# Kernel optimization log

Hardware: AMD Instinct MI355X
Metric: run time of the kernel (lower is better)

The kernel has to match this reference:

```python
import jax, jax.numpy as jnp
import numpy as np

EPS = 1e-7
TWO_PI = 2.0 * np.pi

K = 4096   # num gaussians
R = 8192   # num rays
MAP_SIZE = 100


def setup_inputs() -> dict:
    key = jax.random.key(0)
    k1, k2, k3, k4, k5, k6 = jax.random.split(key, 6)
    pos_raw = jax.random.normal(k1, (K, 2), dtype=jnp.float32)            # pre-sigmoid positions
    conc_raw = jax.random.normal(k2, (K,), dtype=jnp.float32)             # pre-softplus concentration
    scale_raw = 0.1 * jax.random.normal(k3, (K, 2), dtype=jnp.float32)    # log-scales
    rot_raw = jax.random.uniform(k4, (K,), dtype=jnp.float32) * TWO_PI    # rotation angles
    p_rays = jax.random.uniform(k5, (R, 2), dtype=jnp.float32) * MAP_SIZE # ray origins in map coords
    u = jax.random.normal(k6, (R, 2), dtype=jnp.float32)
    u_rays = u / jnp.linalg.norm(u, axis=-1, keepdims=True)               # unit ray directions
    return {"pos_raw": pos_raw, "conc_raw": conc_raw, "scale_raw": scale_raw,
            "rot_raw": rot_raw, "p_rays": p_rays, "u_rays": u_rays,
            "map_size": MAP_SIZE}


def _forward(pos_raw, conc_raw, scale_raw, rot_raw, p_rays, u_rays, map_size):
    # --- per-gaussian activations (GasSplattingModel getters) ---
    pos = jax.nn.sigmoid(pos_raw) * map_size           # (K,2)
    conc = jax.nn.softplus(conc_raw)                   # (K,)
    scale = jnp.exp(scale_raw)                         # (K,2)
    d0 = 1.0 / (scale[:, 0] ** 2 + EPS)                # diag of S^2 inverse
    d1 = 1.0 / (scale[:, 1] ** 2 + EPS)
    c, s = jnp.cos(rot_raw), jnp.sin(rot_raw)
    # Sigma^{-1} = R diag(d0,d1) R^T with R = [[c,-s],[s,c]]  (symmetric 2x2)
    m00 = c * c * d0 + s * s * d1                      # (K,)
    m01 = c * s * (d0 - d1)
    m11 = s * s * d0 + c * c * d1
    M = jnp.stack([m00, m01, m11], axis=0)             # (3,K) quadratic-form coeffs

    u0, u1 = u_rays[:, 0], u_rays[:, 1]
    p0, p1 = p_rays[:, 0], p_rays[:, 1]

    # quadratic-form features per ray, contracted with M via GEMM -> (R,K)
    qu = jnp.stack([u0 * u0, 2.0 * u0 * u1, u1 * u1], axis=1)        # (R,3)
    qp = jnp.stack([p0 * p0, 2.0 * p0 * p1, p1 * p1], axis=1)        # (R,3)
    qup = jnp.stack([u0 * p0, u0 * p1 + u1 * p0, u1 * p1], axis=1)   # (R,3)
    a = qu @ M          # u^T S u      (R,K)
    pSp = qp @ M        # p^T S p      (R,K)
    uSp = qup @ M       # u^T S p      (R,K)

    # S @ mu per gaussian -> (2,K)
    Sm = jnp.stack([m00 * pos[:, 0] + m01 * pos[:, 1],
                    m01 * pos[:, 0] + m11 * pos[:, 1]], axis=0)
    uSm = u_rays @ Sm   # u^T S mu     (R,K)
    pSm = p_rays @ Sm   # p^T S mu     (R,K)
    mSm = pos[:, 0] * Sm[0] + pos[:, 1] * Sm[1]        # mu^T S mu (K,)

    b = uSp - uSm                                      # u^T S (p - mu)
    c0 = pSp - 2.0 * pSm + mSm[None, :]                # (p-mu)^T S (p-mu)

    # closed-form line integral of conc * exp(-0.5 (x-mu)^T S (x-mu)) along ray
    dens = conc[None, :] * jnp.sqrt(TWO_PI / a) * jnp.exp(-0.5 * (c0 - b * b / a))
    return jnp.sum(dens, axis=-1)                      # (R,)


def reference(pos_raw, conc_raw, scale_raw, rot_raw, p_rays, u_rays, map_size):
    return _forward(pos_raw, conc_raw, scale_raw, rot_raw, p_rays, u_rays, map_size)
```

## Files before the change

### kernel.cpp

```cpp
#include <hip/hip_runtime.h>
#include <hip/hip_bf16.h>

#define EPS 1e-07f

#define BLOCK 1024
#define RPB   32
#define NW    (BLOCK/64)

#define SQRT_HALF_LOG2E 0.84932180028801904f
#define LOG2_SQRT_2PI   1.32574806473616588f

typedef float v4f __attribute__((ext_vector_type(4)));

__global__ __launch_bounds__(BLOCK) void fused_splat(
        const float* __restrict__ pos_raw,
        const float* __restrict__ conc_raw,
        const float* __restrict__ scale_raw,
        const float* __restrict__ rot_raw,
        const void*  __restrict__ map_size_p,
        const float* __restrict__ p_rays,
        const float* __restrict__ u_rays,
        float* __restrict__ out,
        int K, int R)
{
    __shared__ float sG[512][6][4];
    __shared__ float psum[NW][RPB];

    const int tid  = threadIdx.x;
    const int lane = tid & 63;
    const int wv   = tid >> 6;
    const int rayl = lane & 31;
    const int half = lane >> 5;
    const int chunk = (wv << 1) | half;

    int ray = blockIdx.x * RPB + rayl;
    if (ray >= R) ray = R - 1;

    unsigned int msbits = *(const unsigned int*)map_size_p;
    float msf = __uint_as_float(msbits);
    const float ms = (msf >= 1e-3f && msf <= 1e9f) ? msf
                                                   : (float)(*(const int*)map_size_p);

    float2 p2 = *(const float2*)(p_rays + 2*ray);
    float2 u2 = *(const float2*)(u_rays + 2*ray);
    const float p0 = p2.x, p1 = p2.y, u0 = u2.x, u1 = u2.y;
    const float qu0  = u0*u0, qu1 = 2.0f*u0*u1, qu2 = u1*u1;
    const float wt   =  SQRT_HALF_LOG2E * (u0*p1 - u1*p0);
    const float su1  =  SQRT_HALF_LOG2E * u1;
    const float nsu0 = -SQRT_HALF_LOG2E * u0;

    float acc = 0.0f;

    const int KH = K >> 1;
    const int CL = KH >> 5;
    const int NG = CL >> 2;

    for (int pass = 0; pass < 2; ++pass) {
        const int kbase = pass * KH;

        __syncthreads();

        for (int k = tid; k < KH; k += BLOCK) {
            const int kg = kbase + k;

            float pr0 = pos_raw[2*kg], pr1 = pos_raw[2*kg+1];
            float pos0 = ms / (1.0f + __expf(-pr0));
            float pos1 = ms / (1.0f + __expf(-pr1));

            float cr = conc_raw[kg];
            float conc = fmaxf(cr, 0.0f) + __logf(1.0f + __expf(-fabsf(cr)));

            float s0 = __expf(scale_raw[2*kg]);
            float s1 = __expf(scale_raw[2*kg+1]);
            float d0 = 1.0f / (s0*s0 + EPS);
            float d1 = 1.0f / (s1*s1 + EPS);

            float rot = rot_raw[kg];
            float c = __cosf(rot), s = __sinf(rot);

            float m00 = c*c*d0 + s*s*d1;
            float m01 = c*s*(d0 - d1);
            float m11 = s*s*d0 + c*c*d1;

            float det    = d0 * d1;
            float invdet = 1.0f / det;
            float cc = __log2f(conc) + LOG2_SQRT_2PI - 0.5f * __log2f(det);

            const int q = k >> 2, e = k & 3;
            sG[q][0][e] = m00 * invdet;
            sG[q][1][e] = m01 * invdet;
            sG[q][2][e] = m11 * invdet;
            sG[q][3][e] = cc;
            sG[q][4][e] = pos0;
            sG[q][5][e] = pos1;
        }
        __syncthreads();

        const int g0 = chunk * NG;
        #pragma unroll 4
        for (int gq = 0; gq < NG; ++gq) {
            const int t4 = g0 + gq;
            v4f M00 = *(const v4f*)&sG[t4][0][0];
            v4f M01 = *(const v4f*)&sG[t4][1][0];
            v4f M11 = *(const v4f*)&sG[t4][2][0];
            v4f CC  = *(const v4f*)&sG[t4][3][0];
            v4f P0  = *(const v4f*)&sG[t4][4][0];
            v4f P1  = *(const v4f*)&sG[t4][5][0];

            #pragma unroll
            for (int g = 0; g < 4; ++g) {
                float a_  = fmaf(qu2, M11[g], fmaf(qu1, M01[g], qu0 * M00[g]));
                float cr_ = fmaf(nsu0, P1[g], fmaf(su1, P0[g], wt));
                float ra_ = __builtin_amdgcn_rsqf(a_);
                float t_  = cr_ * ra_;
                float ar_ = fmaf(-t_, t_, CC[g]);
                float e_  = __builtin_amdgcn_exp2f(ar_);
                acc = fmaf(ra_, e_, acc);
            }
        }
    }

    acc += __shfl_xor(acc, 32, 64);
    if (half == 0) psum[wv][rayl] = acc;
    __syncthreads();

    if (wv == 0 && lane < RPB) {
        float s = 0.0f;
        #pragma unroll
        for (int w = 0; w < NW; ++w) s += psum[w][lane];
        int oray = blockIdx.x * RPB + lane;
        if (oray < R) out[oray] = s;
    }
}

extern "C" void kernel_launch(void* const* d_in, const int* in_sizes, int n_in,
                              void* d_out, int out_size, void* d_ws, size_t ws_size,
                              hipStream_t stream)
{
    const float* pos_raw   = (const float*)d_in[0];
    const float* conc_raw  = (const float*)d_in[1];
    const float* scale_raw = (const float*)d_in[2];
    const float* rot_raw   = (const float*)d_in[3];
    const float* p_rays    = (const float*)d_in[4];
    const float* u_rays    = (const float*)d_in[5];
    const void*  map_size  = d_in[6];

    const int K = in_sizes[1];
    const int R = out_size;

    float* out = (float*)d_out;

    dim3 grid((R + RPB - 1) / RPB);
    fused_splat<<<grid, BLOCK, 0, stream>>>(pos_raw, conc_raw, scale_raw,
                                            rot_raw, map_size,
                                            p_rays, u_rays, out, K, R);
}
```

Measured before the change: 21.03 us.

## Split into precompute kernel and scalar-load splat kernel with K-chunk atomics

The per-gaussian activations move into a separate precompute kernel that writes a padded 4-wide record layout to the workspace and zeroes the output. The main kernel gives one ray per thread, splits K across 64 grid-y chunks, and reads gaussian records through inline-asm scalar loads (s_load) instead of LDS, finishing with an atomicAdd per ray. This removes the per-block redundant activation work, the __syncthreads and the LDS traffic. In exchange it adds a second launch, global atomics, and a full wait on every scalar load that serializes load latency with compute.

```diff
diff --git a/kernel.cpp b/kernel.cpp
--- a/kernel.cpp
+++ b/kernel.cpp
@@ -3,47 +3,94 @@
 
 #define EPS 1e-07f
 
-#define BLOCK 1024
-#define RPB   32
-#define NW    (BLOCK/64)
+#define BLOCK  256
+#define NCH    64
+#define PBLOCK 64
 
 #define SQRT_HALF_LOG2E 0.84932180028801904f
 #define LOG2_SQRT_2PI   1.32574806473616588f
 
 typedef float v4f __attribute__((ext_vector_type(4)));
 
-__global__ __launch_bounds__(BLOCK) void fused_splat(
-        const float* __restrict__ pos_raw,
-        const float* __restrict__ conc_raw,
-        const float* __restrict__ scale_raw,
-        const float* __restrict__ rot_raw,
-        const void*  __restrict__ map_size_p,
-        const float* __restrict__ p_rays,
-        const float* __restrict__ u_rays,
-        float* __restrict__ out,
-        int K, int R)
+__global__ __launch_bounds__(PBLOCK) void precompute_gauss(
+                                 const float* __restrict__ pos_raw,
+                                 const float* __restrict__ conc_raw,
+                                 const float* __restrict__ scale_raw,
+                                 const float* __restrict__ rot_raw,
+                                 const void*  __restrict__ map_size_p,
+                                 float* __restrict__ gG,
+                                 float* __restrict__ out,
+                                 int K, int KPAD, int R)
 {
-    __shared__ float sG[512][6][4];
-    __shared__ float psum[NW][RPB];
+    int k = blockIdx.x * blockDim.x + threadIdx.x;
+    int nthreads = gridDim.x * blockDim.x;
 
-    const int tid  = threadIdx.x;
-    const int lane = tid & 63;
-    const int wv   = tid >> 6;
-    const int rayl = lane & 31;
-    const int half = lane >> 5;
-    const int chunk = (wv << 1) | half;
+    for (int i = k; i < R; i += nthreads) out[i] = 0.0f;
 
-    int ray = blockIdx.x * RPB + rayl;
-    if (ray >= R) ray = R - 1;
+    if (k >= KPAD) return;
+
+    const int q = k >> 2, e = k & 3;
+    float* rec = gG + q * 24;
+
+    if (k >= K) {
+        rec[0  + e] = 1.0f;
+        rec[4  + e] = 0.0f;
+        rec[8  + e] = 1.0f;
+        rec[12 + e] = -1e38f;
+        rec[16 + e] = 0.0f;
+        rec[20 + e] = 0.0f;
+        return;
+    }
 
     unsigned int msbits = *(const unsigned int*)map_size_p;
     float msf = __uint_as_float(msbits);
     const float ms = (msf >= 1e-3f && msf <= 1e9f) ? msf
                                                    : (float)(*(const int*)map_size_p);
 
-    float2 p2 = *(const float2*)(p_rays + 2*ray);
-    float2 u2 = *(const float2*)(u_rays + 2*ray);
+    float pr0 = pos_raw[2*k],  pr1 = pos_raw[2*k+1];
+    float pos0 = ms / (1.0f + __expf(-pr0));
+    float pos1 = ms / (1.0f + __expf(-pr1));
+
+    float cr = conc_raw[k];
+    float conc = fmaxf(cr, 0.0f) + __logf(1.0f + __expf(-fabsf(cr)));
+
+    float s0 = __expf(scale_raw[2*k]);
+    float s1 = __expf(scale_raw[2*k+1]);
+    float d0 = 1.0f / (s0*s0 + EPS);
+    float d1 = 1.0f / (s1*s1 + EPS);
+
+    float rot = rot_raw[k];
+    float c = __cosf(rot), s = __sinf(rot);
+
+    float m00 = c*c*d0 + s*s*d1;
+    float m01 = c*s*(d0 - d1);
+    float m11 = s*s*d0 + c*c*d1;
+
+    float det    = d0 * d1;
+    float invdet = 1.0f / det;
+    float cc = __log2f(conc) + LOG2_SQRT_2PI - 0.5f * __log2f(det);
+
+    rec[0  + e] = m00 * invdet;
+    rec[4  + e] = m01 * invdet;
+    rec[8  + e] = m11 * invdet;
+    rec[12 + e] = cc;
+    rec[16 + e] = pos0;
+    rec[20 + e] = pos1;
+}
+
+__global__ __launch_bounds__(BLOCK) void splat_main(
+        const float* __restrict__ p_rays,
+        const float* __restrict__ u_rays,
+        const float* __restrict__ gG,
+        float* __restrict__ out,
+        int GPC, int R)
+{
+    const int ray = blockIdx.x * BLOCK + threadIdx.x;
+
+    float2 p2 = *(const float2*)(p_rays + 2*min(ray, R-1));
+    float2 u2 = *(const float2*)(u_rays + 2*min(ray, R-1));
     const float p0 = p2.x, p1 = p2.y, u0 = u2.x, u1 = u2.y;
+
     const float qu0  = u0*u0, qu1 = 2.0f*u0*u1, qu2 = u1*u1;
     const float wt   =  SQRT_HALF_LOG2E * (u0*p1 - u1*p0);
     const float su1  =  SQRT_HALF_LOG2E * u1;
@@ -51,86 +98,36 @@
 
     float acc = 0.0f;
 
-    const int KH = K >> 1;
-    const int CL = KH >> 5;
-    const int NG = CL >> 2;
+    const float* gptr = gG + (size_t)blockIdx.y * GPC * 24;
 
-    for (int pass = 0; pass < 2; ++pass) {
-        const int kbase = pass * KH;
+    for (int g = 0; g < GPC; ++g) {
+        v4f M00, M01, M11, CC, P0, P1;
+        asm volatile(
+            "s_load_dwordx4 %0, %6, 0x0\n\t"
+            "s_load_dwordx4 %1, %6, 0x10\n\t"
+            "s_load_dwordx4 %2, %6, 0x20\n\t"
+            "s_load_dwordx4 %3, %6, 0x30\n\t"
+            "s_load_dwordx4 %4, %6, 0x40\n\t"
+            "s_load_dwordx4 %5, %6, 0x50\n\t"
+            "s_waitcnt lgkmcnt(0)"
+            : "=&s"(M00), "=&s"(M01), "=&s"(M11),
+              "=&s"(CC),  "=&s"(P0),  "=&s"(P1)
+            : "s"(gptr));
 
-        __syncthreads();
-
-        for (int k = tid; k < KH; k += BLOCK) {
-            const int kg = kbase + k;
-
-            float pr0 = pos_raw[2*kg], pr1 = pos_raw[2*kg+1];
-            float pos0 = ms / (1.0f + __expf(-pr0));
-            float pos1 = ms / (1.0f + __expf(-pr1));
-
-            float cr = conc_raw[kg];
-            float conc = fmaxf(cr, 0.0f) + __logf(1.0f + __expf(-fabsf(cr)));
-
-            float s0 = __expf(scale_raw[2*kg]);
-            float s1 = __expf(scale_raw[2*kg+1]);
-            float d0 = 1.0f / (s0*s0 + EPS);
-            float d1 = 1.0f / (s1*s1 + EPS);
-
-            float rot = rot_raw[kg];
-            float c = __cosf(rot), s = __sinf(rot);
-
-            float m00 = c*c*d0 + s*s*d1;
-            float m01 = c*s*(d0 - d1);
-            float m11 = s*s*d0 + c*c*d1;
-
-            float det    = d0 * d1;
-            float invdet = 1.0f / det;
-            float cc = __log2f(conc) + LOG2_SQRT_2PI - 0.5f * __log2f(det);
-
-            const int q = k >> 2, e = k & 3;
-            sG[q][0][e] = m00 * invdet;
-            sG[q][1][e] = m01 * invdet;
-            sG[q][2][e] = m11 * invdet;
-            sG[q][3][e] = cc;
-            sG[q][4][e] = pos0;
-            sG[q][5][e] = pos1;
+        #pragma unroll
+        for (int e = 0; e < 4; ++e) {
+            float a_  = fmaf(qu2, M11[e], fmaf(qu1, M01[e], qu0 * M00[e]));
+            float cr_ = fmaf(nsu0, P1[e], fmaf(su1, P0[e], wt));
+            float ra_ = __builtin_amdgcn_rsqf(a_);
+            float t_  = cr_ * ra_;
+            float ar_ = fmaf(-t_, t_, CC[e]);
+            float e_  = __builtin_amdgcn_exp2f(ar_);
+            acc = fmaf(ra_, e_, acc);
         }
-        __syncthreads();
-
-        const int g0 = chunk * NG;
-        #pragma unroll 4
-        for (int gq = 0; gq < NG; ++gq) {
-            const int t4 = g0 + gq;
-            v4f M00 = *(const v4f*)&sG[t4][0][0];
-            v4f M01 = *(const v4f*)&sG[t4][1][0];
-            v4f M11 = *(const v4f*)&sG[t4][2][0];
-            v4f CC  = *(const v4f*)&sG[t4][3][0];
-            v4f P0  = *(const v4f*)&sG[t4][4][0];
-            v4f P1  = *(const v4f*)&sG[t4][5][0];
-
-            #pragma unroll
-            for (int g = 0; g < 4; ++g) {
-                float a_  = fmaf(qu2, M11[g], fmaf(qu1, M01[g], qu0 * M00[g]));
-                float cr_ = fmaf(nsu0, P1[g], fmaf(su1, P0[g], wt));
-                float ra_ = __builtin_amdgcn_rsqf(a_);
-                float t_  = cr_ * ra_;
-                float ar_ = fmaf(-t_, t_, CC[g]);
-                float e_  = __builtin_amdgcn_exp2f(ar_);
-                acc = fmaf(ra_, e_, acc);
-            }
-        }
+        gptr += 24;
     }
 
-    acc += __shfl_xor(acc, 32, 64);
-    if (half == 0) psum[wv][rayl] = acc;
-    __syncthreads();
-
-    if (wv == 0 && lane < RPB) {
-        float s = 0.0f;
-        #pragma unroll
-        for (int w = 0; w < NW; ++w) s += psum[w][lane];
-        int oray = blockIdx.x * RPB + lane;
-        if (oray < R) out[oray] = s;
-    }
+    if (ray < R) atomicAdd(&out[ray], acc);
 }
 
 extern "C" void kernel_launch(void* const* d_in, const int* in_sizes, int n_in,
@@ -148,10 +145,22 @@
     const int K = in_sizes[1];
     const int R = out_size;
 
+    const int ng_tot = (K + 3) / 4;
+    const int GPC    = (ng_tot + NCH - 1) / NCH;
+    const int ng_pad = GPC * NCH;
+    const int KPAD   = ng_pad * 4;
+
     float* out = (float*)d_out;
+    float* gG  = (float*)d_ws;
 
-    dim3 grid((R + RPB - 1) / RPB);
-    fused_splat<<<grid, BLOCK, 0, stream>>>(pos_raw, conc_raw, scale_raw,
-                                            rot_raw, map_size,
-                                            p_rays, u_rays, out, K, R);
+    {
+        dim3 grid((KPAD + PBLOCK - 1) / PBLOCK);
+        precompute_gauss<<<grid, PBLOCK, 0, stream>>>(pos_raw, conc_raw, scale_raw,
+                                                      rot_raw, map_size,
+                                                      gG, out, K, KPAD, R);
+    }
+    {
+        dim3 grid((R + BLOCK - 1) / BLOCK, NCH);
+        splat_main<<<grid, BLOCK, 0, stream>>>(p_rays, u_rays, gG, out, GPC, R);
+    }
 }
```

After: 23.56 us. +12.0%, slower.

## Halve rays per block, split gaussians across 64 chunks with padded LDS records

Applied to the files above, without the earlier changes.

Rays per block drop from 32 to 16, so each wave covers 4 chunks of 16 rays and the block splits gaussians into 64 chunks of 32 per pass. The shared-memory layout is regrouped into padded per-chunk records with a 196-float stride, meant to avoid LDS bank conflicts. The inner loop keeps four independent accumulators for ILP, and a launch-bounds occupancy hint is added. The trade-off is twice as many blocks, so per-block gaussian preprocessing is repeated twice as often, plus an extra shuffle step in the reduction.

```diff
diff --git a/kernel.cpp b/kernel.cpp
--- a/kernel.cpp
+++ b/kernel.cpp
@@ -4,7 +4,10 @@
 #define EPS 1e-07f
 
 #define BLOCK 1024
-#define RPB   32
+#define RPB   16
+#define NCHK  64
+#define GPG   8
+#define CSTRIDE 196
 #define NW    (BLOCK/64)
 
 #define SQRT_HALF_LOG2E 0.84932180028801904f
@@ -12,7 +15,7 @@
 
 typedef float v4f __attribute__((ext_vector_type(4)));
 
-__global__ __launch_bounds__(BLOCK) void fused_splat(
+__global__ __launch_bounds__(BLOCK, 8) void fused_splat(
         const float* __restrict__ pos_raw,
         const float* __restrict__ conc_raw,
         const float* __restrict__ scale_raw,
@@ -23,15 +26,14 @@
         float* __restrict__ out,
         int K, int R)
 {
-    __shared__ float sG[512][6][4];
+    __shared__ float sG[NCHK * CSTRIDE];
     __shared__ float psum[NW][RPB];
 
-    const int tid  = threadIdx.x;
-    const int lane = tid & 63;
-    const int wv   = tid >> 6;
-    const int rayl = lane & 31;
-    const int half = lane >> 5;
-    const int chunk = (wv << 1) | half;
+    const int tid   = threadIdx.x;
+    const int lane  = tid & 63;
+    const int wv    = tid >> 6;
+    const int rayl  = tid & (RPB - 1);
+    const int chunk = tid >> 4;
 
     int ray = blockIdx.x * RPB + rayl;
     if (ray >= R) ray = R - 1;
@@ -49,11 +51,10 @@
     const float su1  =  SQRT_HALF_LOG2E * u1;
     const float nsu0 = -SQRT_HALF_LOG2E * u0;
 
-    float acc = 0.0f;
+    float acc0 = 0.0f, acc1 = 0.0f, acc2 = 0.0f, acc3 = 0.0f;
 
     const int KH = K >> 1;
-    const int CL = KH >> 5;
-    const int NG = CL >> 2;
+    const float* cb = &sG[chunk * CSTRIDE];
 
     for (int pass = 0; pass < 2; ++pass) {
         const int kbase = pass * KH;
@@ -87,41 +88,58 @@
             float cc = __log2f(conc) + LOG2_SQRT_2PI - 0.5f * __log2f(det);
 
             const int q = k >> 2, e = k & 3;
-            sG[q][0][e] = m00 * invdet;
-            sG[q][1][e] = m01 * invdet;
-            sG[q][2][e] = m11 * invdet;
-            sG[q][3][e] = cc;
-            sG[q][4][e] = pos0;
-            sG[q][5][e] = pos1;
+            float* rec = &sG[(q >> 3) * CSTRIDE + (q & 7) * 24];
+            rec[ 0 + e] = m00 * invdet;
+            rec[ 4 + e] = m01 * invdet;
+            rec[ 8 + e] = m11 * invdet;
+            rec[12 + e] = cc;
+            rec[16 + e] = pos0;
+            rec[20 + e] = pos1;
         }
         __syncthreads();
 
-        const int g0 = chunk * NG;
-        #pragma unroll 4
-        for (int gq = 0; gq < NG; ++gq) {
-            const int t4 = g0 + gq;
-            v4f M00 = *(const v4f*)&sG[t4][0][0];
-            v4f M01 = *(const v4f*)&sG[t4][1][0];
-            v4f M11 = *(const v4f*)&sG[t4][2][0];
-            v4f CC  = *(const v4f*)&sG[t4][3][0];
-            v4f P0  = *(const v4f*)&sG[t4][4][0];
-            v4f P1  = *(const v4f*)&sG[t4][5][0];
+        #pragma unroll
+        for (int gq = 0; gq < GPG; ++gq) {
+            const float* g = cb + gq * 24;
+            v4f M00 = *(const v4f*)(g +  0);
+            v4f M01 = *(const v4f*)(g +  4);
+            v4f M11 = *(const v4f*)(g +  8);
+            v4f CC  = *(const v4f*)(g + 12);
+            v4f P0  = *(const v4f*)(g + 16);
+            v4f P1  = *(const v4f*)(g + 20);
 
+            v4f A, CR, RA, AR;
             #pragma unroll
-            for (int g = 0; g < 4; ++g) {
-                float a_  = fmaf(qu2, M11[g], fmaf(qu1, M01[g], qu0 * M00[g]));
-                float cr_ = fmaf(nsu0, P1[g], fmaf(su1, P0[g], wt));
-                float ra_ = __builtin_amdgcn_rsqf(a_);
-                float t_  = cr_ * ra_;
-                float ar_ = fmaf(-t_, t_, CC[g]);
-                float e_  = __builtin_amdgcn_exp2f(ar_);
-                acc = fmaf(ra_, e_, acc);
+            for (int e = 0; e < 4; ++e)
+                A[e]  = fmaf(qu2, M11[e], fmaf(qu1, M01[e], qu0 * M00[e]));
+            #pragma unroll
+            for (int e = 0; e < 4; ++e)
+                CR[e] = fmaf(nsu0, P1[e], fmaf(su1, P0[e], wt));
+            #pragma unroll
+            for (int e = 0; e < 4; ++e)
+                RA[e] = __builtin_amdgcn_rsqf(A[e]);
+            #pragma unroll
+            for (int e = 0; e < 4; ++e) {
+                float t = CR[e] * RA[e];
+                AR[e] = fmaf(-t, t, CC[e]);
+            }
+            {
+                float e0 = __builtin_amdgcn_exp2f(AR[0]);
+                float e1 = __builtin_amdgcn_exp2f(AR[1]);
+                float e2 = __builtin_amdgcn_exp2f(AR[2]);
+                float e3 = __builtin_amdgcn_exp2f(AR[3]);
+                acc0 = fmaf(RA[0], e0, acc0);
+                acc1 = fmaf(RA[1], e1, acc1);
+                acc2 = fmaf(RA[2], e2, acc2);
+                acc3 = fmaf(RA[3], e3, acc3);
             }
         }
     }
 
-    acc += __shfl_xor(acc, 32, 64);
-    if (half == 0) psum[wv][rayl] = acc;
+    float a = (acc0 + acc1) + (acc2 + acc3);
+    a += __shfl_xor(a, 16, 64);
+    a += __shfl_xor(a, 32, 64);
+    if (lane < RPB) psum[wv][lane] = a;
     __syncthreads();
 
     if (wv == 0 && lane < RPB) {
```

Result: slower. 27.39 us (+30.2%).
